# Kernel tuning notes

Hardware: AMD Instinct MI355X
Metric: run time of the kernel (lower is better)

Reference implementation:

```python
import jax, jax.numpy as jnp
from jax import lax
import numpy as np

EPS = 1e-5  # BatchNorm eps (inference mode; dropouts are identity in eval)


def _proj(img, w, g, b, m, v, stride):
    """All-heads Conv2d(3x3, no bias) + BatchNorm (inference) fused across heads.
    img: [B, Cin, H, W]; w: [heads, Cout, Cin, 3, 3]; g/b/m/v: [heads, Cout].
    Returns [B, heads, Cout, N'] (channels-first token layout)."""
    heads, Cout, Cin = w.shape[0], w.shape[1], w.shape[2]
    y = lax.conv_general_dilated(
        img, w.reshape(heads * Cout, Cin, 3, 3),
        window_strides=(stride, stride), padding=[(1, 1), (1, 1)],
        dimension_numbers=('NCHW', 'OIHW', 'NCHW'))
    B = y.shape[0]
    N = y.shape[2] * y.shape[3]
    y = y.reshape(B, heads, Cout, N)
    scale = g / jnp.sqrt(v + EPS)               # [heads, Cout]
    shift = b - m * scale
    return y * scale[None, :, :, None] + shift[None, :, :, None]


def reference(x, y, w_conv, bn_gamma, bn_beta, bn_mean, bn_var, w_out1, w_out2, h, w):
    B, N, C = x.shape
    xi = x.reshape(B, h, w, C).transpose(0, 3, 1, 2)  # b (h w) c -> b c h w
    yi = y.reshape(B, h, w, C).transpose(0, 3, 1, 2)
    scale_attn = C ** -0.5

    def P(i, img, stride):
        return _proj(img, w_conv[i], bn_gamma[i], bn_beta[i], bn_mean[i], bn_var[i], stride)

    # torch: query1(x), query2(y), key1(y), key2(x), value1(y), value2(x)
    Q1 = P(0, xi, 2)  # [B,h,C,Nq]
    Q2 = P(1, yi, 2)
    K1 = P(2, yi, 2)
    K2 = P(3, xi, 2)
    V1 = P(4, yi, 1)  # [B,h,C,Nv]
    V2 = P(5, xi, 1)

    # channel-attention: scores are [B, heads, C, C], softmax over last axis
    s1 = jnp.einsum('bhcn,bhdn->bhcd', Q2, K1) * scale_attn
    s2 = jnp.einsum('bhcn,bhdn->bhcd', Q1, K2) * scale_attn
    p1 = jax.nn.softmax(s1, axis=-1)
    p2 = jax.nn.softmax(s2, axis=-1)

    # context [B,heads,C,Nv] -> mean over heads -> [B,Nv,C]
    c1 = jnp.einsum('bhcd,bhdn->bhcn', p1, V1).mean(axis=1).transpose(0, 2, 1)
    c2 = jnp.einsum('bhcd,bhdn->bhcn', p2, V2).mean(axis=1).transpose(0, 2, 1)

    o1 = c1 @ w_out1.T  # Linear(dim_in, dim_out, bias=False)
    o2 = c2 @ w_out2.T
    return o1, o2


def setup_inputs() -> dict:
    B, C, HEADS, H, W = 8, 256, 4, 64, 64
    key = jax.random.key(0)
    ks = jax.random.split(key, 9)
    conv_std = 1.0 / np.sqrt(C * 9)
    lin_std = 1.0 / np.sqrt(C)
    return {
        'x': jax.random.normal(ks[0], (B, H * W, C), jnp.float32),
        'y': jax.random.normal(ks[1], (B, H * W, C), jnp.float32),
        'w_conv': jax.random.normal(ks[2], (6, HEADS, C, C, 3, 3), jnp.float32) * conv_std,
        'bn_gamma': jax.random.uniform(ks[3], (6, HEADS, C), jnp.float32, 0.5, 1.5),
        'bn_beta': jax.random.normal(ks[4], (6, HEADS, C), jnp.float32) * 0.1,
        'bn_mean': jax.random.normal(ks[5], (6, HEADS, C), jnp.float32) * 0.1,
        'bn_var': jax.random.uniform(ks[6], (6, HEADS, C), jnp.float32, 0.5, 1.5),
        'w_out1': jax.random.normal(ks[7], (C, C), jnp.float32) * lin_std,
        'w_out2': jax.random.normal(ks[8], (C, C), jnp.float32) * lin_std,
        'h': H,
        'w': W,
    }
```

## Files before the change

### kernel.cpp

```cpp
#include <hip/hip_runtime.h>
#include <stdint.h>

typedef __bf16 bf16_t;
typedef __bf16 bf16x8 __attribute__((ext_vector_type(8)));
typedef float f32x4 __attribute__((ext_vector_type(4)));

#define EPSBN 1e-5f

#define OFF_XP   ((size_t)0)
#define SZ_IMG   ((size_t)8*4356*256*2)
#define OFF_YP   (OFF_XP + SZ_IMG)
#define OFF_WQS  (OFF_YP + SZ_IMG)
#define SZ_WQS   ((size_t)4*1024*2304*2)
#define OFF_WVT  (OFF_WQS + SZ_WQS)
#define SZ_WVT   ((size_t)2*2304*1024*2)
#define OFF_W1B  (OFF_WVT + SZ_WVT)
#define SZ_WO    ((size_t)65536*2)
#define OFF_W2B  (OFF_W1B + SZ_WO)
#define OFF_SHQ  (OFF_W2B + SZ_WO)
#define SZ_SHQ   ((size_t)4096*4)
#define OFF_SHV  (OFF_SHQ + SZ_SHQ)
#define SZ_SHV   ((size_t)2048*4)
#define OFF_QK   (OFF_SHV + SZ_SHV)
#define SZ_QK    ((size_t)4*8*1024*1024*2)
#define OFF_S    (OFF_QK + SZ_QK)
#define SZ_S     ((size_t)2*8*4*65536*4)
#define OFF_PT   (OFF_S + SZ_S)
#define SZ_PT    ((size_t)2*8*4*65536*2)
#define OFF_A1   (OFF_PT + SZ_PT)
#define SZ_A1    ((size_t)2*8*256*1024*2)
#define OFF_WEFF (OFF_A1 + SZ_A1)
#define SZ_WEFF  ((size_t)2*8*256*2304*2)
#define OFF_BIAS (OFF_WEFF + SZ_WEFF)
#define SZ_BIAS  ((size_t)2*8*256*4)
#define WS_NEED  (OFF_BIAS + SZ_BIAS)

__device__ __forceinline__ void gload16(const bf16_t* g, bf16_t* l) {
  __builtin_amdgcn_global_load_lds(
      (const __attribute__((address_space(1))) void*)g,
      (__attribute__((address_space(3))) void*)l,
      16, 0, 0);
}

__device__ __forceinline__ int lb_off0() { return ((threadIdx.x >> 6)    ) * 512; }
__device__ __forceinline__ int lb_off1() { return ((threadIdx.x >> 6) + 4) * 512; }

#define SBAR0 __builtin_amdgcn_sched_barrier(0)

template<int BSRC>
__device__ __forceinline__ void gemm_core(
    const bf16_t* __restrict__ A, int ldA,
    const bf16_t* __restrict__ B, int ldB,
    int m0, int n0, int KT, f32x4 acc[4][4])
{
  __shared__ bf16_t lA[2][4096];
  __shared__ bf16_t lB[2][4096];
  const int tid  = threadIdx.x;
  const int lane = tid & 63;
  const int wv   = tid >> 6;
  const int wr   = wv >> 1, wc = wv & 1;
  const int r4   = lane >> 2;
  const int k8   = (lane & 3) * 8;

  const bf16_t* gA0 = A + (size_t)(m0 + (wv    )*16 + r4) * ldA + k8;
  const bf16_t* gA1 = A + (size_t)(m0 + (wv + 4)*16 + r4) * ldA + k8;
  const int la0 = (wv    ) * 512;
  const int la1 = (wv + 4) * 512;
  const bf16_t* gB0 = B + (size_t)(n0 + (wv    )*16 + r4) * ldB + k8;
  const bf16_t* gB1 = B + (size_t)(n0 + (wv + 4)*16 + r4) * ldB + k8;
  (void)BSRC;

#pragma unroll
  for (int i = 0; i < 4; ++i)
#pragma unroll
    for (int j = 0; j < 4; ++j)
      acc[i][j] = f32x4{0.f, 0.f, 0.f, 0.f};

  const int lr = lane & 15;
  const int lk = (lane >> 4) * 8;
  int aidx[4], bidx[4];
#pragma unroll
  for (int f = 0; f < 4; ++f) {
    aidx[f] = (wr*64 + f*16 + lr)*32 + lk;
    bidx[f] = (wc*64 + f*16 + lr)*32 + lk;
  }

  auto stage = [&](int bufp, int kt) {
    const int kb = kt * 32;
    gload16(gA0 + kb, &lA[bufp][la0]);
    gload16(gA1 + kb, &lA[bufp][la1]);
    gload16(gB0 + kb, &lB[bufp][lb_off0()]);
    gload16(gB1 + kb, &lB[bufp][lb_off1()]);
  };

  stage(0, 0);
  __syncthreads();
  int buf = 0;
  for (int kt = 0; kt < KT; ++kt) {
    if (kt + 1 < KT) stage(buf ^ 1, kt + 1);
    bf16x8 av[4], bvv[4];
#pragma unroll
    for (int f = 0; f < 4; ++f) av[f]  = *(const bf16x8*)&lA[buf][aidx[f]];
#pragma unroll
    for (int f = 0; f < 4; ++f) bvv[f] = *(const bf16x8*)&lB[buf][bidx[f]];
#pragma unroll
    for (int i = 0; i < 4; ++i)
#pragma unroll
      for (int j = 0; j < 4; ++j)
        acc[i][j] = __builtin_amdgcn_mfma_f32_16x16x32_bf16(av[i], bvv[j], acc[i][j], 0, 0, 0);
    __syncthreads();
    buf ^= 1;
  }
}

template<int STRIDE>
__device__ __forceinline__ void conv_m201_core(
    const bf16_t* __restrict__ A, const bf16_t* __restrict__ img,
    int m0, int n0, f32x4 acc[8][4])
{
  __shared__ bf16_t lA[2][2][8192];
  __shared__ bf16_t lB[2][2][8192];
  const int tid  = threadIdx.x;
  const int lane = tid & 63;
  const int w    = tid >> 6;
  const int wm   = w >> 2;
  const int wn   = w & 3;
  const int wh   = wn >> 1;
  const int wn1  = wn & 1;

#pragma unroll
  for (int f = 0; f < 8; ++f)
#pragma unroll
    for (int c = 0; c < 4; ++c)
      acc[f][c] = f32x4{0.f, 0.f, 0.f, 0.f};

  const int srow = tid >> 3;
  const int swz  = ((tid & 7) ^ (srow & 7)) * 8;
  const bf16_t* gAsrc = A + (size_t)(m0 + srow) * 2304 + swz;
  const bf16_t* gBsrc[4];
#pragma unroll
  for (int h = 0; h < 2; ++h)
#pragma unroll
    for (int c = 0; c < 2; ++c) {
      const int tok = n0 + h*128 + c*64 + srow;
      int px;
      if (STRIDE == 1) px = (tok >> 6)*66 + (tok & 63);
      else             px = ((tok >> 5)*2)*66 + (tok & 31)*2;
      gBsrc[h*2 + c] = img + (size_t)px*256 + swz;
    }

  auto stageA = [&](int T1, int h) {
    bf16_t* dst = &lA[T1 & 1][h][0] + tid*8;
    const bf16_t* src = gAsrc + (size_t)(h*128)*2304 + T1*64;
    gload16(src, dst);
    gload16(src + (size_t)64*2304, dst + 4096);
  };
  auto stageB = [&](int T1, int h) {
    const int tap = T1 >> 2;
    const int ky  = (tap >= 6) ? 2 : ((tap >= 3) ? 1 : 0);
    const int kx  = tap - ky*3;
    const int ps  = (ky*66 + kx)*256 + (T1 & 3)*64;
    bf16_t* dst = &lB[T1 & 1][h][0] + tid*8;
    gload16(gBsrc[h*2 + 0] + ps, dst);
    gload16(gBsrc[h*2 + 1] + ps, dst + 4096);
  };

  const int rb  = (lane & 15) * 64;
  const int l7  = lane & 7;
  const int g4  = lane >> 4;
  int rs[2];
  rs[0] = ((    g4) ^ l7) * 8;
  rs[1] = ((4 + g4) ^ l7) * 8;

  stageA(0, 0); stageB(0, 0); stageA(0, 1); stageB(0, 1);
  SBAR0;
  asm volatile("s_waitcnt vmcnt(0)" ::: "memory");
  SBAR0;
  __builtin_amdgcn_s_barrier();

#define MFMA2(F, J, AV) do {                                                  \
    acc[F][J] = __builtin_amdgcn_mfma_f32_16x16x32_bf16(AV[0], bvs[(J)>>1][(J)&1][0], acc[F][J], 0, 0, 0); \
    acc[F][J] = __builtin_amdgcn_mfma_f32_16x16x32_bf16(AV[1], bvs[(J)>>1][(J)&1][1], acc[F][J], 0, 0, 0); \
  } while (0)

  for (int T = 0; T < 36; ++T) {
    const int buf = T & 1;
    const bf16_t* pa = &lA[buf][wm][0];
    const bf16_t* pb = &lB[buf][wh][0];
    bf16x8 avl[4][2], avh[4][2], bvs[2][2][2];
    const bool nt = (T + 1 < 36);

#pragma unroll
    for (int j = 0; j < 2; ++j)
#pragma unroll
      for (int kh = 0; kh < 2; ++kh)
        bvs[0][j][kh] = *(const bf16x8*)(pb + (wn1*4096 + j*1024 + rb + rs[kh]));
    SBAR0;
#pragma unroll
    for (int i = 0; i < 4; ++i)
#pragma unroll
      for (int kh = 0; kh < 2; ++kh)
        avl[i][kh] = *(const bf16x8*)(pa + (i*1024 + rb + rs[kh]));
    SBAR0;
#pragma unroll
    for (int j = 0; j < 2; ++j)
#pragma unroll
      for (int kh = 0; kh < 2; ++kh)
        bvs[1][j][kh] = *(const bf16x8*)(pb + (wn1*4096 + (2+j)*1024 + rb + rs[kh]));
    SBAR0;
#pragma unroll
    for (int i = 0; i < 4; ++i)
#pragma unroll
      for (int kh = 0; kh < 2; ++kh)
        avh[i][kh] = *(const bf16x8*)(pa + ((4+i)*1024 + rb + rs[kh]));
    SBAR0;
    if (nt) { stageA(T+1, 0); stageB(T+1, 0); stageA(T+1, 1); stageB(T+1, 1); }
    SBAR0;

    __builtin_amdgcn_s_setprio(1);
    asm volatile("s_waitcnt lgkmcnt(15)" ::: "memory"); SBAR0;
    MFMA2(0,0,avl[0]); MFMA2(0,1,avl[0]);
    MFMA2(1,0,avl[1]); MFMA2(1,1,avl[1]);
    SBAR0;
    asm volatile("s_waitcnt lgkmcnt(14)" ::: "memory"); SBAR0;
    MFMA2(2,0,avl[2]); MFMA2(2,1,avl[2]);
    SBAR0;
    asm volatile("s_waitcnt lgkmcnt(12)" ::: "memory"); SBAR0;
    MFMA2(3,0,avl[3]); MFMA2(3,1,avl[3]);
    SBAR0;
    asm volatile("s_waitcnt lgkmcnt(8)" ::: "memory"); SBAR0;
#pragma unroll
    for (int i = 0; i < 4; ++i) { MFMA2(i,2,avl[i]); MFMA2(i,3,avl[i]); }
    SBAR0;
    asm volatile("s_waitcnt lgkmcnt(6)" ::: "memory"); SBAR0;
    MFMA2(4,0,avh[0]); MFMA2(4,1,avh[0]);
    SBAR0;
    asm volatile("s_waitcnt lgkmcnt(4)" ::: "memory"); SBAR0;
    MFMA2(5,0,avh[1]); MFMA2(5,1,avh[1]);
    SBAR0;
    asm volatile("s_waitcnt lgkmcnt(2)" ::: "memory"); SBAR0;
    MFMA2(6,0,avh[2]); MFMA2(6,1,avh[2]);
    SBAR0;
    asm volatile("s_waitcnt lgkmcnt(0)" ::: "memory"); SBAR0;
    MFMA2(7,0,avh[3]); MFMA2(7,1,avh[3]);
#pragma unroll
    for (int i = 0; i < 4; ++i) { MFMA2(4+i,2,avh[i]); MFMA2(4+i,3,avh[i]); }
    __builtin_amdgcn_s_setprio(0);
    SBAR0;
    asm volatile("s_waitcnt vmcnt(0)" ::: "memory");
    SBAR0;
    __builtin_amdgcn_s_barrier();
  }
#undef MFMA2
}

__global__ __launch_bounds__(512, 1) void k_conv_qk7(const bf16_t* __restrict__ wqs,
    const bf16_t* __restrict__ xp, const bf16_t* __restrict__ yp,
    bf16_t* __restrict__ qk, const float* __restrict__ shq)
{
  const int n  = blockIdx.x;
  const int b  = n & 7;
  const int r1 = n >> 3;
  const int ci = r1 & 3;
  const int r2 = r1 >> 2;
  const int nt = r2 & 3;
  const int mt = r2 >> 2;
  const int m0 = mt*256, n0 = nt*256;
  const bf16_t* A = wqs + (size_t)ci * 1024 * 2304;
  const bf16_t* img = (((ci == 0) | (ci == 3)) ? xp : yp) + (size_t)b*4356*256;
  f32x4 acc[8][4];
  conv_m201_core<2>(A, img, m0, n0, acc);

  bf16_t* out = qk + (size_t)(ci*8 + b) * 1024 * 1024;
  const float* sh = shq + ci*1024;
  const int lane = threadIdx.x & 63, w = threadIdx.x >> 6;
  const int wm = w >> 2, wn = w & 3;
#pragma unroll
  for (int f = 0; f < 8; ++f) {
    const int row0 = m0 + wm*128 + f*16 + ((lane >> 4) << 2);
    const f32x4 s4 = *(const f32x4*)&sh[row0];
#pragma unroll
    for (int c = 0; c < 4; ++c) {
      const int col = n0 + wn*64 + c*16 + (lane & 15);
#pragma unroll
      for (int r = 0; r < 4; ++r)
        out[(size_t)(row0 + r)*1024 + col] = (bf16_t)(acc[f][c][r] + s4[r]);
    }
  }
}

__global__ __launch_bounds__(512, 1) void k_conv_out7(const bf16_t* __restrict__ weff,
    const bf16_t* __restrict__ xp, const bf16_t* __restrict__ yp,
    const float* __restrict__ bias, float* __restrict__ dout)
{
  const int n  = blockIdx.x;
  const int b  = n & 7;
  const int r1 = n >> 3;
  const int br = r1 & 1;
  const int nt = r1 >> 1;
  const int n0 = nt*256;
  const bf16_t* A = weff + (size_t)(br*8 + b)*589824;
  const bf16_t* img = ((br == 0) ? yp : xp) + (size_t)b*4356*256;
  f32x4 acc[8][4];
  conv_m201_core<1>(A, img, 0, n0, acc);

  float* outp = dout + (size_t)br*8388608 + (size_t)b*1048576;
  const float* bp = bias + (size_t)(br*8 + b)*256;
  const int lane = threadIdx.x & 63, w = threadIdx.x >> 6;
  const int wm = w >> 2, wn = w & 3;
#pragma unroll
  for (int f = 0; f < 8; ++f) {
    const int e0 = wm*128 + f*16 + ((lane >> 4) << 2);
    const f32x4 bv4 = *(const f32x4*)&bp[e0];
#pragma unroll
    for (int c = 0; c < 4; ++c) {
      const int tok = n0 + wn*64 + c*16 + (lane & 15);
      f32x4 v = acc[f][c] + bv4;
      *(f32x4*)&outp[(size_t)tok*256 + e0] = v;
    }
  }
}

__global__ __launch_bounds__(256) void k_pack(const float* __restrict__ x, const float* __restrict__ y,
                                              bf16_t* __restrict__ xp, bf16_t* __restrict__ yp)
{
  const int t   = threadIdx.x;
  const int pix = blockIdx.x*4 + (t >> 6);
  const int c4  = (t & 63) * 4;
  const int b   = blockIdx.y;
  const int im  = blockIdx.z;
  const int i = pix / 66, j = pix - i*66;
  const float* src = im ? y : x;
  bf16_t* dst = im ? yp : xp;
  float4 v = make_float4(0.f, 0.f, 0.f, 0.f);
  if (i >= 1 && i <= 64 && j >= 1 && j <= 64)
    v = *(const float4*)&src[((size_t)b*4096 + (size_t)(i-1)*64 + (j-1))*256 + c4];
  bf16_t o4[4] = {(bf16_t)v.x, (bf16_t)v.y, (bf16_t)v.z, (bf16_t)v.w};
  *(uint64_t*)&dst[((size_t)b*4356 + pix)*256 + c4] = *(const uint64_t*)o4;
}

__global__ __launch_bounds__(256) void k_prep_wq(const float* __restrict__ wcv,
    const float* __restrict__ g, const float* __restrict__ be,
    const float* __restrict__ mu, const float* __restrict__ va,
    bf16_t* __restrict__ wqs, float* __restrict__ shq)
{
  const int blk = blockIdx.x;
  __shared__ float lw[2304];
  const float* src = wcv + (size_t)blk * 2304;
  for (int t = threadIdx.x; t < 2304; t += 256) lw[t] = src[t];
  const float sc = g[blk] * rsqrtf(va[blk] + EPSBN);
  if (threadIdx.x == 0) shq[blk] = be[blk] - mu[blk]*sc;
  __syncthreads();
  bf16_t* dst = wqs + (size_t)blk * 2304;
  for (int t = threadIdx.x; t < 2304; t += 256) {
    const int tap = t >> 8, c = t & 255;
    dst[t] = (bf16_t)(lw[c*9 + tap] * sc);
  }
}

__global__ __launch_bounds__(256) void k_prep_wv(const float* __restrict__ wcv,
    const float* __restrict__ g, const float* __restrict__ va,
    bf16_t* __restrict__ wvT)
{
  const int cch = blockIdx.x;
  const int h = blockIdx.y >> 2, dc = blockIdx.y & 3;
  const int br = blockIdx.z;
  __shared__ float lw[64][72];
  __shared__ float lsc[64];
  const int ci = 4 + br;
  const int c0 = cch*8, d0 = dc*64;
  for (int e = threadIdx.x; e < 64*72; e += 256) {
    const int dd = e / 72, q = e - dd*72;
    lw[dd][q] = wcv[(size_t)(ci*1024 + h*256 + d0 + dd)*2304 + c0*9 + q];
  }
  if (threadIdx.x < 64) {
    const int bnIdx = ci*1024 + h*256 + d0 + threadIdx.x;
    lsc[threadIdx.x] = g[bnIdx] * rsqrtf(va[bnIdx] + EPSBN);
  }
  __syncthreads();
  for (int e = threadIdx.x; e < 72*64; e += 256) {
    const int kq = e >> 6, dd = e & 63;
    const int cc = kq / 9, tap = kq - cc*9;
    const int kp = tap*256 + c0 + cc;
    wvT[(size_t)br*2359296 + (size_t)kp*1024 + h*256 + d0 + dd] =
        (bf16_t)(lw[dd][cc*9 + tap] * lsc[dd]);
  }
}

__global__ __launch_bounds__(256) void k_small(const float* __restrict__ w1, const float* __restrict__ w2,
    const float* __restrict__ g, const float* __restrict__ be,
    const float* __restrict__ mu, const float* __restrict__ va,
    bf16_t* __restrict__ w1b, bf16_t* __restrict__ w2b, float* __restrict__ shv)
{
  const int idx = blockIdx.x*256 + threadIdx.x;
  if (idx < 65536) {
    w1b[idx] = (bf16_t)w1[idx];
  } else if (idx < 131072) {
    w2b[idx - 65536] = (bf16_t)w2[idx - 65536];
  } else if (idx < 133120) {
    const int t = idx - 131072;
    const int bnIdx = 4096 + t;
    const float sc = g[bnIdx] * rsqrtf(va[bnIdx] + EPSBN);
    shv[t] = be[bnIdx] - mu[bnIdx]*sc;
  }
}

__global__ __launch_bounds__(256) void k_gemm_s(const bf16_t* __restrict__ qk, float* __restrict__ sb)
{
  const int bx = blockIdx.x, by = blockIdx.y, br = blockIdx.z;
  const int mt = bx >> 1, nt = bx & 1;
  const int b = by >> 2, h = by & 3;
  const int ai = (br == 0) ? 1 : 0;
  const int bi = (br == 0) ? 2 : 3;
  const bf16_t* A  = qk + ((size_t)(ai*8 + b)*1024 + h*256) * 1024;
  const bf16_t* Bp = qk + ((size_t)(bi*8 + b)*1024 + h*256) * 1024;
  f32x4 acc[4][4];
  gemm_core<0>(A, 1024, Bp, 1024, mt*128, nt*128, 32, acc);

  float* out = sb + ((size_t)(br*8 + b)*4 + h) * 65536;
  const int lane = threadIdx.x & 63, wv = threadIdx.x >> 6;
  const int wr = wv >> 1, wc = wv & 1;
#pragma unroll
  for (int i = 0; i < 4; ++i) {
    const int row0 = mt*128 + wr*64 + i*16 + ((lane >> 4) << 2);
#pragma unroll
    for (int j = 0; j < 4; ++j) {
      const int col = nt*128 + wc*64 + j*16 + (lane & 15);
#pragma unroll
      for (int r = 0; r < 4; ++r)
        out[(size_t)(row0 + r)*256 + col] = acc[i][j][r];
    }
  }
}

__global__ __launch_bounds__(256) void k_softmax(const float* __restrict__ sb, bf16_t* __restrict__ pt)
{
  const int cc = blockIdx.x;
  const int bh = blockIdx.y;
  const int br = blockIdx.z;
  const size_t base = ((size_t)br*32 + bh) * 65536;
  __shared__ bf16_t lp[32][256];
  const int tid = threadIdx.x, lane = tid & 63, wv = tid >> 6;
  for (int r = 0; r < 8; ++r) {
    const int row = wv*8 + r;
    const float* srow = sb + base + (size_t)(cc*32 + row)*256;
    f32x4 v = ((const f32x4*)srow)[lane];
    v *= 0.0625f;
    float m = fmaxf(fmaxf(v[0], v[1]), fmaxf(v[2], v[3]));
#pragma unroll
    for (int o = 32; o; o >>= 1) m = fmaxf(m, __shfl_xor(m, o));
    const float e0 = __expf(v[0]-m), e1 = __expf(v[1]-m), e2 = __expf(v[2]-m), e3 = __expf(v[3]-m);
    float s = e0+e1+e2+e3;
#pragma unroll
    for (int o = 32; o; o >>= 1) s += __shfl_xor(s, o);
    const float inv = 0.25f / s;
    lp[row][lane*4+0] = (bf16_t)(e0*inv);
    lp[row][lane*4+1] = (bf16_t)(e1*inv);
    lp[row][lane*4+2] = (bf16_t)(e2*inv);
    lp[row][lane*4+3] = (bf16_t)(e3*inv);
  }
  __syncthreads();
  bf16_t* dst = pt + base;
  for (int it = 0; it < 32; ++it) {
    const int idx = it*256 + tid;
    const int d = idx >> 5, c = idx & 31;
    dst[(size_t)d*256 + cc*32 + c] = lp[c][d];
  }
}

__global__ __launch_bounds__(256) void k_gemm_a(const bf16_t* __restrict__ w1b, const bf16_t* __restrict__ w2b,
    const bf16_t* __restrict__ pt, bf16_t* __restrict__ a1)
{
  const int bx = blockIdx.x, by = blockIdx.y, br = blockIdx.z;
  const int mt = bx >> 1, nt = bx & 1;
  const int b = by >> 2, h = by & 3;
  const bf16_t* A  = br ? w2b : w1b;
  const bf16_t* Bp = pt + ((size_t)(br*8 + b)*4 + h) * 65536;
  f32x4 acc[4][4];
  gemm_core<0>(A, 256, Bp, 256, mt*128, nt*128, 8, acc);

  bf16_t* out = a1 + (size_t)(br*8 + b)*262144 + h*256;
  const int lane = threadIdx.x & 63, wv = threadIdx.x >> 6;
  const int wr = wv >> 1, wc = wv & 1;
#pragma unroll
  for (int i = 0; i < 4; ++i) {
    const int row0 = mt*128 + wr*64 + i*16 + ((lane >> 4) << 2);
#pragma unroll
    for (int j = 0; j < 4; ++j) {
      const int col = nt*128 + wc*64 + j*16 + (lane & 15);
#pragma unroll
      for (int r = 0; r < 4; ++r)
        out[(size_t)(row0 + r)*1024 + col] = (bf16_t)acc[i][j][r];
    }
  }
}

__global__ __launch_bounds__(256) void k_bias(const bf16_t* __restrict__ a1,
    const float* __restrict__ shv, float* __restrict__ bias)
{
  const int wv = threadIdx.x >> 6, lane = threadIdx.x & 63;
  const int e = blockIdx.x*4 + wv;
  const int b = blockIdx.y, br = blockIdx.z;
  const bf16_t* row = a1 + ((size_t)(br*8 + b)*256 + e)*1024;
  const float* sv = shv + br*1024;
  float acc = 0.f;
#pragma unroll
  for (int t = 0; t < 16; ++t) {
    const int idx = t*64 + lane;
    acc += (float)row[idx] * sv[idx];
  }
#pragma unroll
  for (int o = 32; o; o >>= 1) acc += __shfl_xor(acc, o);
  if (lane == 0) bias[(size_t)(br*8 + b)*256 + e] = acc;
}

__global__ __launch_bounds__(256) void k_gemm_weff(const bf16_t* __restrict__ a1,
    const bf16_t* __restrict__ wvT, bf16_t* __restrict__ weff)
{
  const int bx = blockIdx.x, b = blockIdx.y, br = blockIdx.z;
  const int mt = bx / 18, nt = bx - mt*18;
  const bf16_t* A  = a1 + (size_t)(br*8 + b)*262144;
  const bf16_t* Bp = wvT + (size_t)br*2359296;
  f32x4 acc[4][4];
  gemm_core<0>(A, 1024, Bp, 1024, mt*128, nt*128, 32, acc);

  bf16_t* out = weff + (size_t)(br*8 + b)*589824;
  const int lane = threadIdx.x & 63, wv = threadIdx.x >> 6;
  const int wr = wv >> 1, wc = wv & 1;
#pragma unroll
  for (int i = 0; i < 4; ++i) {
    const int row0 = mt*128 + wr*64 + i*16 + ((lane >> 4) << 2);
#pragma unroll
    for (int j = 0; j < 4; ++j) {
      const int col = nt*128 + wc*64 + j*16 + (lane & 15);
#pragma unroll
      for (int r = 0; r < 4; ++r)
        out[(size_t)(row0 + r)*2304 + col] = (bf16_t)acc[i][j][r];
    }
  }
}

extern "C" void kernel_launch(void* const* d_in, const int* in_sizes, int n_in,
                              void* d_out, int out_size, void* d_ws, size_t ws_size,
                              hipStream_t stream)
{
  (void)in_sizes; (void)n_in; (void)out_size;
  const float* x   = (const float*)d_in[0];
  const float* y   = (const float*)d_in[1];
  const float* wcv = (const float*)d_in[2];
  const float* bg  = (const float*)d_in[3];
  const float* bb  = (const float*)d_in[4];
  const float* bm  = (const float*)d_in[5];
  const float* bvv = (const float*)d_in[6];
  const float* w1  = (const float*)d_in[7];
  const float* w2  = (const float*)d_in[8];
  float* out = (float*)d_out;
  char* ws = (char*)d_ws;
  if (ws_size < WS_NEED) return;

  bf16_t* xp   = (bf16_t*)(ws + OFF_XP);
  bf16_t* yp   = (bf16_t*)(ws + OFF_YP);
  bf16_t* wqs  = (bf16_t*)(ws + OFF_WQS);
  bf16_t* wvT  = (bf16_t*)(ws + OFF_WVT);
  bf16_t* w1b  = (bf16_t*)(ws + OFF_W1B);
  bf16_t* w2b  = (bf16_t*)(ws + OFF_W2B);
  float*  shq  = (float*)(ws + OFF_SHQ);
  float*  shv  = (float*)(ws + OFF_SHV);
  bf16_t* qk   = (bf16_t*)(ws + OFF_QK);
  float*  sb   = (float*)(ws + OFF_S);
  bf16_t* pt   = (bf16_t*)(ws + OFF_PT);
  bf16_t* a1   = (bf16_t*)(ws + OFF_A1);
  bf16_t* weff = (bf16_t*)(ws + OFF_WEFF);
  float*  bias = (float*)(ws + OFF_BIAS);

  k_pack     <<<dim3(1089, 8, 2), 256, 0, stream>>>(x, y, xp, yp);
  k_prep_wq  <<<dim3(4096), 256, 0, stream>>>(wcv, bg, bb, bm, bvv, wqs, shq);
  k_prep_wv  <<<dim3(32, 16, 2), 256, 0, stream>>>(wcv, bg, bvv, wvT);
  k_small    <<<dim3(520), 256, 0, stream>>>(w1, w2, bg, bb, bm, bvv, w1b, w2b, shv);
  k_conv_qk7 <<<dim3(512), 512, 0, stream>>>(wqs, xp, yp, qk, shq);
  k_gemm_s   <<<dim3(4, 32, 2), 256, 0, stream>>>(qk, sb);
  k_softmax  <<<dim3(8, 32, 2), 256, 0, stream>>>(sb, pt);
  k_gemm_a   <<<dim3(4, 32, 2), 256, 0, stream>>>(w1b, w2b, pt, a1);
  k_bias     <<<dim3(64, 8, 2), 256, 0, stream>>>(a1, shv, bias);
  k_gemm_weff<<<dim3(36, 8, 2), 256, 0, stream>>>(a1, wvT, weff);
  k_conv_out7<<<dim3(256), 512, 0, stream>>>(weff, xp, yp, bias, out);
}
```

Baseline: 328.1 us.

## Fuse channel-attention score GEMM with softmax into one kernel

Replaces the separate score GEMM (writing fp32 scores to workspace) and softmax kernel with a single kernel. Each block computes full 128x256 score rows with MFMA, then does the row max and sum reduction in registers and LDS, and writes transposed bf16 probabilities directly. This removes the fp32 score round trip through memory and one kernel launch. The cost is fewer blocks (128 instead of 256) with 512 threads each, so parallelism is lower.

New measurement: 318.1 us. -3.0%, faster.

```diff
diff --git a/kernel.cpp b/kernel.cpp
--- a/kernel.cpp
+++ b/kernel.cpp
@@ -321,6 +321,190 @@
   }
 }
 
+__global__ __launch_bounds__(512, 1) void k_sp(const bf16_t* __restrict__ qk,
+                                               bf16_t* __restrict__ pt)
+{
+  const int mt = blockIdx.x;
+  const int by = blockIdx.y;
+  const int br = blockIdx.z;
+  const int b = by >> 2, h = by & 3;
+  const int ai = (br == 0) ? 1 : 0;
+  const int bi = (br == 0) ? 2 : 3;
+  const bf16_t* A = qk + ((size_t)(ai*8 + b)*1024 + h*256 + mt*128) * 1024;
+  const bf16_t* B = qk + ((size_t)(bi*8 + b)*1024 + h*256) * 1024;
+
+  __shared__ bf16_t lA[2][4096];
+  __shared__ bf16_t lB[2][8192];
+  __shared__ float red[4][128];
+
+  const int tid = threadIdx.x, lane = tid & 63, w = tid >> 6;
+  const int wm = w >> 2, wn = w & 3;
+
+  f32x4 acc[4][4];
+#pragma unroll
+  for (int i = 0; i < 4; ++i)
+#pragma unroll
+    for (int j = 0; j < 4; ++j)
+      acc[i][j] = f32x4{0.f, 0.f, 0.f, 0.f};
+
+  const int srow = tid >> 2;
+  const int ksX  = (tid & 3) ^ ((tid >> 3) & 3);
+  const bf16_t* gA  = A + (size_t)srow*1024 + ksX*8;
+  const bf16_t* gB0 = B + (size_t)srow*1024 + ksX*8;
+  const bf16_t* gB1 = B + (size_t)(srow + 128)*1024 + ksX*8;
+
+  auto stage = [&](int p, int buf) {
+    gload16(gA  + p*32, &lA[buf][0] + tid*8);
+    bf16_t* dB = &lB[buf][0] + tid*8;
+    gload16(gB0 + p*32, dB);
+    gload16(gB1 + p*32, dB + 4096);
+  };
+
+  const int lr    = lane & 15;
+  const int slotS = (lane >> 4) ^ ((lane & 6) >> 1);
+  int offA[4], offB[4];
+#pragma unroll
+  for (int f = 0; f < 4; ++f) offA[f] = (wm*64 + f*16 + lr)*32 + slotS*8;
+#pragma unroll
+  for (int c = 0; c < 4; ++c) offB[c] = (wn*64 + c*16 + lr)*32 + slotS*8;
+
+  stage(0, 0);
+  SBAR0;
+  asm volatile("s_waitcnt vmcnt(0)" ::: "memory");
+  SBAR0;
+  __builtin_amdgcn_s_barrier();
+  SBAR0;
+
+  for (int p = 0; p < 32; ++p) {
+    const int buf = p & 1;
+    const bf16_t* pA = &lA[buf][0];
+    const bf16_t* pB = &lB[buf][0];
+    bf16x8 av[4], bv[4];
+    av[0] = *(const bf16x8*)(pA + offA[0]);
+    av[1] = *(const bf16x8*)(pA + offA[1]);
+#pragma unroll
+    for (int c = 0; c < 4; ++c) bv[c] = *(const bf16x8*)(pB + offB[c]);
+    SBAR0;
+    av[2] = *(const bf16x8*)(pA + offA[2]);
+    av[3] = *(const bf16x8*)(pA + offA[3]);
+    SBAR0;
+    if (p + 1 < 32) stage(p + 1, buf ^ 1);
+    SBAR0;
+    __builtin_amdgcn_s_setprio(1);
+    asm volatile("s_waitcnt lgkmcnt(2)" ::: "memory");
+    SBAR0;
+#pragma unroll
+    for (int f = 0; f < 2; ++f)
+#pragma unroll
+      for (int c = 0; c < 4; ++c)
+        acc[f][c] = __builtin_amdgcn_mfma_f32_16x16x32_bf16(av[f], bv[c], acc[f][c], 0, 0, 0);
+    SBAR0;
+    asm volatile("s_waitcnt lgkmcnt(0)" ::: "memory");
+    SBAR0;
+#pragma unroll
+    for (int f = 2; f < 4; ++f)
+#pragma unroll
+      for (int c = 0; c < 4; ++c)
+        acc[f][c] = __builtin_amdgcn_mfma_f32_16x16x32_bf16(av[f], bv[c], acc[f][c], 0, 0, 0);
+    __builtin_amdgcn_s_setprio(0);
+    SBAR0;
+    asm volatile("s_waitcnt vmcnt(0)" ::: "memory");
+    SBAR0;
+    __builtin_amdgcn_s_barrier();
+    SBAR0;
+  }
+
+  const int g = lane >> 4;
+  const int rowb = wm*64 + (lane >> 4)*4;
+
+  f32x4 mr[4];
+#pragma unroll
+  for (int i = 0; i < 4; ++i) {
+    f32x4 m01, m23;
+#pragma unroll
+    for (int r = 0; r < 4; ++r) {
+      m01[r] = fmaxf(acc[i][0][r], acc[i][1][r]);
+      m23[r] = fmaxf(acc[i][2][r], acc[i][3][r]);
+      mr[i][r] = fmaxf(m01[r], m23[r]);
+    }
+  }
+#pragma unroll
+  for (int o = 1; o < 16; o <<= 1)
+#pragma unroll
+    for (int i = 0; i < 4; ++i)
+#pragma unroll
+      for (int r = 0; r < 4; ++r)
+        mr[i][r] = fmaxf(mr[i][r], __shfl_xor(mr[i][r], o));
+  if ((lane & 15) == 0) {
+#pragma unroll
+    for (int i = 0; i < 4; ++i)
+#pragma unroll
+      for (int r = 0; r < 4; ++r)
+        red[wn][rowb + i*16 + r] = mr[i][r];
+  }
+  __syncthreads();
+  f32x4 mf[4];
+#pragma unroll
+  for (int i = 0; i < 4; ++i)
+#pragma unroll
+    for (int r = 0; r < 4; ++r) {
+      const int row = rowb + i*16 + r;
+      mf[i][r] = fmaxf(fmaxf(red[0][row], red[1][row]), fmaxf(red[2][row], red[3][row]));
+    }
+  __syncthreads();
+
+  f32x4 sr[4];
+#pragma unroll
+  for (int i = 0; i < 4; ++i) {
+    sr[i] = f32x4{0.f, 0.f, 0.f, 0.f};
+#pragma unroll
+    for (int j = 0; j < 4; ++j)
+#pragma unroll
+      for (int r = 0; r < 4; ++r) {
+        const float e = __expf((acc[i][j][r] - mf[i][r]) * 0.0625f);
+        acc[i][j][r] = e;
+        sr[i][r] += e;
+      }
+  }
+#pragma unroll
+  for (int o = 1; o < 16; o <<= 1)
+#pragma unroll
+    for (int i = 0; i < 4; ++i)
+#pragma unroll
+      for (int r = 0; r < 4; ++r)
+        sr[i][r] += __shfl_xor(sr[i][r], o);
+  if ((lane & 15) == 0) {
+#pragma unroll
+    for (int i = 0; i < 4; ++i)
+#pragma unroll
+      for (int r = 0; r < 4; ++r)
+        red[wn][rowb + i*16 + r] = sr[i][r];
+  }
+  __syncthreads();
+  f32x4 inv[4];
+#pragma unroll
+  for (int i = 0; i < 4; ++i)
+#pragma unroll
+    for (int r = 0; r < 4; ++r) {
+      const int row = rowb + i*16 + r;
+      inv[i][r] = 0.25f / (red[0][row] + red[1][row] + red[2][row] + red[3][row]);
+    }
+
+  bf16_t* out = pt + ((size_t)(br*8 + b)*4 + h) * 65536;
+#pragma unroll
+  for (int i = 0; i < 4; ++i) {
+    const int c0 = mt*128 + wm*64 + i*16 + (g << 2);
+#pragma unroll
+    for (int j = 0; j < 4; ++j) {
+      const int d = wn*64 + j*16 + (lane & 15);
+      bf16_t o4[4];
+#pragma unroll
+      for (int r = 0; r < 4; ++r) o4[r] = (bf16_t)(acc[i][j][r] * inv[i][r]);
+      *(uint64_t*)&out[(size_t)d*256 + c0] = *(const uint64_t*)o4;
+    }
+  }
+}
+
 __global__ __launch_bounds__(256) void k_pack(const float* __restrict__ x, const float* __restrict__ y,
                                               bf16_t* __restrict__ xp, bf16_t* __restrict__ yp)
 {
@@ -405,69 +589,6 @@
   }
 }
 
-__global__ __launch_bounds__(256) void k_gemm_s(const bf16_t* __restrict__ qk, float* __restrict__ sb)
-{
-  const int bx = blockIdx.x, by = blockIdx.y, br = blockIdx.z;
-  const int mt = bx >> 1, nt = bx & 1;
-  const int b = by >> 2, h = by & 3;
-  const int ai = (br == 0) ? 1 : 0;
-  const int bi = (br == 0) ? 2 : 3;
-  const bf16_t* A  = qk + ((size_t)(ai*8 + b)*1024 + h*256) * 1024;
-  const bf16_t* Bp = qk + ((size_t)(bi*8 + b)*1024 + h*256) * 1024;
-  f32x4 acc[4][4];
-  gemm_core<0>(A, 1024, Bp, 1024, mt*128, nt*128, 32, acc);
-
-  float* out = sb + ((size_t)(br*8 + b)*4 + h) * 65536;
-  const int lane = threadIdx.x & 63, wv = threadIdx.x >> 6;
-  const int wr = wv >> 1, wc = wv & 1;
-#pragma unroll
-  for (int i = 0; i < 4; ++i) {
-    const int row0 = mt*128 + wr*64 + i*16 + ((lane >> 4) << 2);
-#pragma unroll
-    for (int j = 0; j < 4; ++j) {
-      const int col = nt*128 + wc*64 + j*16 + (lane & 15);
-#pragma unroll
-      for (int r = 0; r < 4; ++r)
-        out[(size_t)(row0 + r)*256 + col] = acc[i][j][r];
-    }
-  }
-}
-
-__global__ __launch_bounds__(256) void k_softmax(const float* __restrict__ sb, bf16_t* __restrict__ pt)
-{
-  const int cc = blockIdx.x;
-  const int bh = blockIdx.y;
-  const int br = blockIdx.z;
-  const size_t base = ((size_t)br*32 + bh) * 65536;
-  __shared__ bf16_t lp[32][256];
-  const int tid = threadIdx.x, lane = tid & 63, wv = tid >> 6;
-  for (int r = 0; r < 8; ++r) {
-    const int row = wv*8 + r;
-    const float* srow = sb + base + (size_t)(cc*32 + row)*256;
-    f32x4 v = ((const f32x4*)srow)[lane];
-    v *= 0.0625f;
-    float m = fmaxf(fmaxf(v[0], v[1]), fmaxf(v[2], v[3]));
-#pragma unroll
-    for (int o = 32; o; o >>= 1) m = fmaxf(m, __shfl_xor(m, o));
-    const float e0 = __expf(v[0]-m), e1 = __expf(v[1]-m), e2 = __expf(v[2]-m), e3 = __expf(v[3]-m);
-    float s = e0+e1+e2+e3;
-#pragma unroll
-    for (int o = 32; o; o >>= 1) s += __shfl_xor(s, o);
-    const float inv = 0.25f / s;
-    lp[row][lane*4+0] = (bf16_t)(e0*inv);
-    lp[row][lane*4+1] = (bf16_t)(e1*inv);
-    lp[row][lane*4+2] = (bf16_t)(e2*inv);
-    lp[row][lane*4+3] = (bf16_t)(e3*inv);
-  }
-  __syncthreads();
-  bf16_t* dst = pt + base;
-  for (int it = 0; it < 32; ++it) {
-    const int idx = it*256 + tid;
-    const int d = idx >> 5, c = idx & 31;
-    dst[(size_t)d*256 + cc*32 + c] = lp[c][d];
-  }
-}
-
 __global__ __launch_bounds__(256) void k_gemm_a(const bf16_t* __restrict__ w1b, const bf16_t* __restrict__ w2b,
     const bf16_t* __restrict__ pt, bf16_t* __restrict__ a1)
 {
@@ -567,7 +688,6 @@
   float*  shq  = (float*)(ws + OFF_SHQ);
   float*  shv  = (float*)(ws + OFF_SHV);
   bf16_t* qk   = (bf16_t*)(ws + OFF_QK);
-  float*  sb   = (float*)(ws + OFF_S);
   bf16_t* pt   = (bf16_t*)(ws + OFF_PT);
   bf16_t* a1   = (bf16_t*)(ws + OFF_A1);
   bf16_t* weff = (bf16_t*)(ws + OFF_WEFF);
@@ -578,8 +698,7 @@
   k_prep_wv  <<<dim3(32, 16, 2), 256, 0, stream>>>(wcv, bg, bvv, wvT);
   k_small    <<<dim3(520), 256, 0, stream>>>(w1, w2, bg, bb, bm, bvv, w1b, w2b, shv);
   k_conv_qk7 <<<dim3(512), 512, 0, stream>>>(wqs, xp, yp, qk, shq);
-  k_gemm_s   <<<dim3(4, 32, 2), 256, 0, stream>>>(qk, sb);
-  k_softmax  <<<dim3(8, 32, 2), 256, 0, stream>>>(sb, pt);
+  k_sp       <<<dim3(2, 32, 2), 512, 0, stream>>>(qk, pt);
   k_gemm_a   <<<dim3(4, 32, 2), 256, 0, stream>>>(w1b, w2b, pt, a1);
   k_bias     <<<dim3(64, 8, 2), 256, 0, stream>>>(a1, shv, bias);
   k_gemm_weff<<<dim3(36, 8, 2), 256, 0, stream>>>(a1, wvT, weff);
```
